# Kernel tuning notes

Hardware: AMD Instinct MI355X
Metric: run time of the kernel (lower is better)

Reference implementation:

```python
import jax, jax.numpy as jnp
import numpy as np

EPS = 1e-6        # eigenvalue clamp for numerical safety (matrices are well-conditioned by construction)
MOMENTUM = 0.1    # init kwarg


def _sym_apply(X, fn):
    """Apply a spectral function to a batch of symmetric matrices via eigh."""
    w, V = jnp.linalg.eigh(X)
    w = jnp.maximum(w, EPS)
    return jnp.einsum('...ij,...j,...kj->...ik', V, fn(w), V)


def sqrtm(X):
    return _sym_apply(X, jnp.sqrt)


def invsqrtm(X):
    return _sym_apply(X, lambda w: 1.0 / jnp.sqrt(w))


def logm(X):
    return _sym_apply(X, jnp.log)


def expm_sym(X):
    w, V = jnp.linalg.eigh(X)
    return jnp.einsum('...ij,...j,...kj->...ik', V, jnp.exp(w), V)


def powm(X, t):
    return _sym_apply(X, lambda w: w ** t)


def congr_neg(X, G):
    """CongrG(X, G, 'neg') = G^{-1/2} X G^{-1/2}, broadcast over batch dims of X."""
    Gi = invsqrtm(G)
    return jnp.einsum('ij,...jk,kl->...il', Gi, X, Gi)


def bary_geom(Xm):
    """Karcher (Frechet) mean of SPD matrices Xm: (N, n, n).
    One Karcher-flow step initialized at the arithmetic mean (SPDNet-BN convention)."""
    G = jnp.mean(Xm, axis=0)
    Gs, Gi = sqrtm(G), invsqrtm(G)
    L = logm(jnp.einsum('ij,bjk,kl->bil', Gi, Xm, Gi))   # log-maps at G
    return Gs @ expm_sym(jnp.mean(L, axis=0)) @ Gs


def geodesic(A, B, t):
    """SPD geodesic from A toward B at time t: A^{1/2} (A^{-1/2} B A^{-1/2})^t A^{1/2}."""
    As, Ai = sqrtm(A), invsqrtm(A)
    return As @ powm(Ai @ B @ Ai, t) @ As


def setup_inputs() -> dict:
    key = jax.random.key(0)
    N, T, V, M, n = 32, 64, 25, 2, 16
    A = jax.random.normal(key, (N, T, V, M, n, n), dtype=jnp.float32)
    # SPD construction: A A^T / n + 0.5 I  (min eigenvalue >= 0.5)
    X = jnp.einsum('...ij,...kj->...ik', A, A) / n + 0.5 * jnp.eye(n, dtype=jnp.float32)
    running_mean = jnp.eye(n, dtype=jnp.float32)  # torch.eye(n) in __init__
    return {"X": X, "running_mean": running_mean}


def reference(X, running_mean):
    N, T, V, M, n, _ = X.shape
    Xf = X.reshape(N, T * V * M, n, n)
    X_mean = jnp.mean(Xf, axis=1)                      # (N, n, n) per-sample arithmetic mean
    mean = bary_geom(X_mean)                           # (n, n) Karcher mean over batch
    new_running_mean = geodesic(running_mean, mean, MOMENTUM)  # no_grad EMA in torch
    X_centered = congr_neg(Xf, mean)                   # mean^{-1/2} X mean^{-1/2}
    return X_centered.reshape(N, T, V, M, n, n), new_running_mean
```

## Files before the change

kernel.cpp:

```cpp
#include <hip/hip_runtime.h>
#include <math.h>

#define NS     32
#define BBATCH 3200
#define NMAT   102400
#define EPSC   1e-6f
#define ST     20
#define IX(i,j) ((i)*ST+(j))
#define MSZ    (16*ST)

#define PART_O 0
#define XM_O   131072
#define GS_O   139264
#define GI_O   139520
#define L_O    139776
#define MEAN_O 147968
#define WI_O   148224
#define RS_O   148480
#define RI_O   148736


__device__ __forceinline__ void g2l(const float* __restrict__ g, float* l, int t) {
  if (t < 64) {
    int i = t >> 2, j0 = (t & 3) << 2;
    *(float4*)&l[IX(i, j0)] = *(const float4*)&g[i * 16 + j0];
  }
  __syncthreads();
}

__device__ __forceinline__ void l2g(const float* l, float* __restrict__ g, int t) {
  if (t < 64) {
    int i = t >> 2, j0 = (t & 3) << 2;
    *(float4*)&g[i * 16 + j0] = *(const float4*)&l[IX(i, j0)];
  }
  __syncthreads();
}

__device__ __forceinline__ void mm(const float* A, const float* B, float* C, int t) {
  if (t < 64) {
    int i = t >> 2, j0 = (t & 3) << 2;
    float4 acc = make_float4(0.f, 0.f, 0.f, 0.f);
    #pragma unroll
    for (int k = 0; k < 16; ++k) {
      float a = A[IX(i, k)];
      const float4 b = *(const float4*)&B[IX(k, j0)];
      acc.x += a * b.x; acc.y += a * b.y; acc.z += a * b.z; acc.w += a * b.w;
    }
    *(float4*)&C[IX(i, j0)] = acc;
  }
  __syncthreads();
}

__device__ __forceinline__ void mad_diag(float* C, float s, float d, int t) {
  if (t < 64) {
    int i = t >> 2, j0 = (t & 3) << 2;
    float4 p = *(float4*)&C[IX(i, j0)];
    p.x *= s; p.y *= s; p.z *= s; p.w *= s;
    if (i == j0) p.x += d; else if (i == j0 + 1) p.y += d;
    else if (i == j0 + 2) p.z += d; else if (i == j0 + 3) p.w += d;
    *(float4*)&C[IX(i, j0)] = p;
  }
  __syncthreads();
}

__device__ __forceinline__ void set_scaled_I(float* C, float d, int t) {
  if (t < 64) {
    int i = t >> 2, j0 = (t & 3) << 2;
    float4 p = make_float4(0.f, 0.f, 0.f, 0.f);
    if (i == j0) p.x = d; else if (i == j0 + 1) p.y = d;
    else if (i == j0 + 2) p.z = d; else if (i == j0 + 3) p.w = d;
    *(float4*)&C[IX(i, j0)] = p;
  }
  __syncthreads();
}

__device__ __forceinline__ void symmetrize(float* A, int t) {
  float4 v = make_float4(0.f, 0.f, 0.f, 0.f);
  if (t < 64) {
    int i = t >> 2, j0 = (t & 3) << 2;
    float4 a = *(float4*)&A[IX(i, j0)];
    v.x = 0.5f * (a.x + A[IX(j0,     i)]);
    v.y = 0.5f * (a.y + A[IX(j0 + 1, i)]);
    v.z = 0.5f * (a.z + A[IX(j0 + 2, i)]);
    v.w = 0.5f * (a.w + A[IX(j0 + 3, i)]);
  }
  __syncthreads();
  if (t < 64) {
    int i = t >> 2, j0 = (t & 3) << 2;
    *(float4*)&A[IX(i, j0)] = v;
  }
  __syncthreads();
}

__device__ __forceinline__ float trace16(const float* A) {
  float tr = 0.f;
  #pragma unroll
  for (int k = 0; k < 16; ++k) tr += A[IX(k, k)];
  return tr;
}

#define NS_IT 8
__device__ void ns_sqrtm(const float* A, float* Y0, float* Y1, float* Z0, float* Z1,
                         float* P, int t, float** pS, float** pZ) {
  float c = trace16(A) * (1.f / 16.f);
  float ic = 1.f / c;
  if (t < 64) {
    int i = t >> 2, j0 = (t & 3) << 2;
    float4 a = *(const float4*)&A[IX(i, j0)];
    a.x *= ic; a.y *= ic; a.z *= ic; a.w *= ic;
    *(float4*)&Y0[IX(i, j0)] = a;
    float4 z = make_float4(0.f, 0.f, 0.f, 0.f);
    if (i == j0) z.x = 1.f; else if (i == j0 + 1) z.y = 1.f;
    else if (i == j0 + 2) z.z = 1.f; else if (i == j0 + 3) z.w = 1.f;
    *(float4*)&Z0[IX(i, j0)] = z;
  }
  __syncthreads();
  float *Y = Y0, *Yn = Y1, *Z = Z0, *Zn = Z1;
  for (int it = 0; it < NS_IT; ++it) {
    mm(Z, Y, P, t);
    mad_diag(P, -0.5f, 1.5f, t);
    mm(Y, P, Yn, t);
    mm(P, Z, Zn, t);
    float* tp = Y; Y = Yn; Yn = tp;
    tp = Z; Z = Zn; Zn = tp;
  }
  float sc = sqrtf(c), isc = 1.f / sc;
  if (t < 64) {
    int i = t >> 2, j0 = (t & 3) << 2;
    float4 y = *(float4*)&Y[IX(i, j0)];
    y.x *= sc; y.y *= sc; y.z *= sc; y.w *= sc;
    *(float4*)&Y[IX(i, j0)] = y;
    float4 z = *(float4*)&Z[IX(i, j0)];
    z.x *= isc; z.y *= isc; z.z *= isc; z.w *= isc;
    *(float4*)&Z[IX(i, j0)] = z;
  }
  __syncthreads();
  *pS = Y; *pZ = Z;
}

#define LOG_M 12
__device__ void logm_taylor(float* S, float* L, float* R0, float* R1, int t) {
  mad_diag(S, 1.f, -1.f, t);
  float am = ((LOG_M & 1) ? 1.f : -1.f) / (float)LOG_M;
  set_scaled_I(R0, am, t);
  float *R = R0, *Rn = R1;
  for (int j = LOG_M - 1; j >= 1; --j) {
    mm(S, R, Rn, t);
    float aj = ((j & 1) ? 1.f : -1.f) / (float)j;
    mad_diag(Rn, 1.f, aj, t);
    float* tp = R; R = Rn; Rn = tp;
  }
  mm(S, R, L, t);
}

#define EXP_M 10
__device__ float* expm_taylor(const float* K, float* R0, float* R1, int t) {
  set_scaled_I(R0, 1.f, t);
  float *R = R0, *Rn = R1;
  for (int j = EXP_M; j >= 1; --j) {
    mm(K, R, Rn, t);
    mad_diag(Rn, 1.f / (float)j, 1.f, t);
    float* tp = R; R = Rn; Rn = tp;
  }
  return R;
}


__global__ __launch_bounds__(256) void k_part(const float* __restrict__ X, float* __restrict__ ws) {
  int b = blockIdx.x >> 4;
  int c = blockIdx.x & 15;
  int t = threadIdx.x;
  int e4 = t & 63;
  int r  = t >> 6;
  const float4* X4 = (const float4*)X;
  float4 s = make_float4(0.f, 0.f, 0.f, 0.f);
  long mbase = (long)b * BBATCH + c * 200;
  for (int i = r; i < 200; i += 4) {
    float4 v = X4[(mbase + i) * 64 + e4];
    s.x += v.x; s.y += v.y; s.z += v.z; s.w += v.w;
  }
  __shared__ float4 red[256];
  red[t] = s;
  __syncthreads();
  if (t < 64) {
    float4 a = red[t], b1 = red[t + 64], c1 = red[t + 128], d = red[t + 192];
    float4 o;
    o.x = a.x + b1.x + c1.x + d.x;
    o.y = a.y + b1.y + c1.y + d.y;
    o.z = a.z + b1.z + c1.z + d.z;
    o.w = a.w + b1.w + c1.w + d.w;
    ((float4*)(ws + PART_O))[(long)blockIdx.x * 64 + t] = o;
  }
}

__global__ __launch_bounds__(256) void k_xm(float* __restrict__ ws) {
  int b = blockIdx.x, t = threadIdx.x;
  float a = 0.f;
  for (int c = 0; c < 16; ++c) a += ws[PART_O + (b * 16 + c) * 256 + t];
  ws[XM_O + b * 256 + t] = a * (1.f / BBATCH);
}

__global__ __launch_bounds__(64) void k_prep(const float* __restrict__ rm, float* __restrict__ ws) {
  __shared__ __align__(16) float A[MSZ], Y0[MSZ], Y1[MSZ], Z0[MSZ], Z1[MSZ], P[MSZ];
  int t = threadIdx.x;
  if (blockIdx.x == 0) {
    if (t < 64) {
      int i = t >> 2, j0 = (t & 3) << 2;
      float4 a = make_float4(0.f, 0.f, 0.f, 0.f);
      for (int b = 0; b < NS; ++b) {
        float4 v = *(const float4*)&ws[XM_O + b * 256 + i * 16 + j0];
        a.x += v.x; a.y += v.y; a.z += v.z; a.w += v.w;
      }
      float s = 1.f / NS;
      a.x *= s; a.y *= s; a.z *= s; a.w *= s;
      *(float4*)&A[IX(i, j0)] = a;
    }
    __syncthreads();
  } else {
    g2l(rm, A, t);
  }
  float *S, *Z;
  ns_sqrtm(A, Y0, Y1, Z0, Z1, P, t, &S, &Z);
  l2g(S, ws + (blockIdx.x == 0 ? GS_O : RS_O), t);
  l2g(Z, ws + (blockIdx.x == 0 ? GI_O : RI_O), t);
}

__global__ __launch_bounds__(64) void k_logmap(float* __restrict__ ws) {
  __shared__ __align__(16) float Gi[MSZ], Xb[MSZ], S[MSZ], T[MSZ], R0[MSZ], R1[MSZ];
  int b = blockIdx.x, t = threadIdx.x;
  g2l(ws + GI_O, Gi, t);
  g2l(ws + XM_O + b * 256, Xb, t);
  mm(Gi, Xb, T, t);
  mm(T, Gi, S, t);
  symmetrize(S, t);
  logm_taylor(S, T, R0, R1, t);
  l2g(T, ws + L_O + b * 256, t);
}

__global__ __launch_bounds__(64) void k_mean2(float* __restrict__ ws) {
  __shared__ __align__(16) float K[MSZ], Gs[MSZ], T1[MSZ], T2[MSZ], R0[MSZ], R1[MSZ], P[MSZ];
  int t = threadIdx.x;
  if (t < 64) {
    int i = t >> 2, j0 = (t & 3) << 2;
    float4 a = make_float4(0.f, 0.f, 0.f, 0.f);
    for (int b = 0; b < NS; ++b) {
      float4 v = *(const float4*)&ws[L_O + b * 256 + i * 16 + j0];
      a.x += v.x; a.y += v.y; a.z += v.z; a.w += v.w;
    }
    float s = 1.f / NS;
    a.x *= s; a.y *= s; a.z *= s; a.w *= s;
    *(float4*)&K[IX(i, j0)] = a;
  }
  __syncthreads();
  float* E = expm_taylor(K, R0, R1, t);
  g2l(ws + GS_O, Gs, t);
  mm(Gs, E, T1, t);
  mm(T1, Gs, T2, t);
  symmetrize(T2, t);
  l2g(T2, ws + MEAN_O, t);
  float *S, *Z;
  ns_sqrtm(T2, R0, R1, T1, K, P, t, &S, &Z);
  l2g(Z, ws + WI_O, t);
}

__global__ __launch_bounds__(256) void k_center(const float* __restrict__ X,
                                                const float* __restrict__ ws,
                                                float* __restrict__ out) {
  __shared__ __align__(16) float B0[MSZ], B1[MSZ], B2[MSZ], B3[MSZ], B4[MSZ];
  __shared__ __align__(16) float Xs[4 * MSZ];
  __shared__ __align__(16) float Ts[4 * MSZ];
  __shared__ __align__(16) float Wsm[MSZ];
  int t = threadIdx.x;

  if (blockIdx.x == 0) {
    g2l(ws + RI_O, B0, t);
    g2l(ws + MEAN_O, B1, t);
    mm(B0, B1, B2, t);
    mm(B2, B0, B1, t);
    symmetrize(B1, t);
    float c = trace16(B1) * (1.f / 16.f);
    mad_diag(B1, 1.f / c, 0.f, t);
    logm_taylor(B1, B2, B3, B4, t);
    mad_diag(B2, 0.1f, 0.f, t);
    float* Ep = expm_taylor(B2, B3, B4, t);
    float s = expf(0.1f * logf(c));
    mad_diag(Ep, s, 0.f, t);
    g2l(ws + RS_O, B1, t);
    mm(B1, Ep, B2, t);
    mm(B2, B1, B4, t);
    l2g(B4, out + (size_t)NMAT * 256, t);
  } else {
    long m0 = (long)(blockIdx.x - 1) * 4;
    Wsm[(t >> 4) * ST + (t & 15)] = ws[WI_O + t];
    const float4* X4 = (const float4*)X;
    float4 xv = X4[m0 * 64 + t];
    int mm_ = t >> 6;
    int l  = t & 63;
    int i  = l >> 2;
    int j0 = (l & 3) << 2;
    *(float4*)&Xs[mm_ * MSZ + i * ST + j0] = xv;
    __syncthreads();
    float4 a = make_float4(0.f, 0.f, 0.f, 0.f);
    #pragma unroll
    for (int k = 0; k < 16; ++k) {
      float x = Xs[mm_ * MSZ + i * ST + k];
      const float4 wv = *(const float4*)&Wsm[k * ST + j0];
      a.x += x * wv.x; a.y += x * wv.y; a.z += x * wv.z; a.w += x * wv.w;
    }
    *(float4*)&Ts[mm_ * MSZ + i * ST + j0] = a;
    __syncthreads();
    float4 y = make_float4(0.f, 0.f, 0.f, 0.f);
    #pragma unroll
    for (int k = 0; k < 16; ++k) {
      float w = Wsm[i * ST + k];
      const float4 tv = *(const float4*)&Ts[mm_ * MSZ + k * ST + j0];
      y.x += w * tv.x; y.y += w * tv.y; y.z += w * tv.z; y.w += w * tv.w;
    }
    ((float4*)out)[m0 * 64 + t] = y;
  }
}

extern "C" void kernel_launch(void* const* d_in, const int* in_sizes, int n_in,
                              void* d_out, int out_size, void* d_ws, size_t ws_size,
                              hipStream_t stream) {
  (void)in_sizes; (void)n_in; (void)out_size; (void)ws_size;
  const float* X  = (const float*)d_in[0];
  const float* rm = (const float*)d_in[1];
  float* out = (float*)d_out;
  float* ws  = (float*)d_ws;

  k_part   <<<dim3(512),   dim3(256), 0, stream>>>(X, ws);
  k_xm     <<<dim3(32),    dim3(256), 0, stream>>>(ws);
  k_prep   <<<dim3(2),     dim3(64),  0, stream>>>(rm, ws);
  k_logmap <<<dim3(32),    dim3(64),  0, stream>>>(ws);
  k_mean2  <<<dim3(1),     dim3(64),  0, stream>>>(ws);
  k_center <<<dim3(25601), dim3(256), 0, stream>>>(X, ws, out);
}
```

Before: 246.4 us.

## Fuse spectral stages into one wave-synchronous kernel and restructure centering

Merges the four small serial kernels (mean reduction, sqrt prep, log-maps, Karcher mean, geodesic) into a single 256-thread block. Each wavefront works independently and uses LDS waitcnt in place of block barriers, which cuts launch and barrier overhead on the serial critical path. Newton-Schulz and Taylor iteration counts are reduced, which may hurt accuracy. The centering kernel now processes 16 matrices per block with register-held W rows and prefetch of the next X matrix.

```diff
diff --git a/kernel.cpp b/kernel.cpp
--- a/kernel.cpp
+++ b/kernel.cpp
@@ -4,162 +4,152 @@
 #define NS     32
 #define BBATCH 3200
 #define NMAT   102400
-#define EPSC   1e-6f
 #define ST     20
 #define IX(i,j) ((i)*ST+(j))
 #define MSZ    (16*ST)
+#define SLAB   324
 
 #define PART_O 0
 #define XM_O   131072
-#define GS_O   139264
-#define GI_O   139520
-#define L_O    139776
-#define MEAN_O 147968
-#define WI_O   148224
-#define RS_O   148480
-#define RI_O   148736
-
-
-__device__ __forceinline__ void g2l(const float* __restrict__ g, float* l, int t) {
-  if (t < 64) {
-    int i = t >> 2, j0 = (t & 3) << 2;
-    *(float4*)&l[IX(i, j0)] = *(const float4*)&g[i * 16 + j0];
-  }
-  __syncthreads();
-}
-
-__device__ __forceinline__ void l2g(const float* l, float* __restrict__ g, int t) {
-  if (t < 64) {
-    int i = t >> 2, j0 = (t & 3) << 2;
-    *(float4*)&g[i * 16 + j0] = *(const float4*)&l[IX(i, j0)];
-  }
-  __syncthreads();
-}
-
-__device__ __forceinline__ void mm(const float* A, const float* B, float* C, int t) {
-  if (t < 64) {
-    int i = t >> 2, j0 = (t & 3) << 2;
-    float4 acc = make_float4(0.f, 0.f, 0.f, 0.f);
-    #pragma unroll
-    for (int k = 0; k < 16; ++k) {
-      float a = A[IX(i, k)];
-      const float4 b = *(const float4*)&B[IX(k, j0)];
-      acc.x += a * b.x; acc.y += a * b.y; acc.z += a * b.z; acc.w += a * b.w;
-    }
-    *(float4*)&C[IX(i, j0)] = acc;
-  }
-  __syncthreads();
-}
-
-__device__ __forceinline__ void mad_diag(float* C, float s, float d, int t) {
-  if (t < 64) {
-    int i = t >> 2, j0 = (t & 3) << 2;
-    float4 p = *(float4*)&C[IX(i, j0)];
-    p.x *= s; p.y *= s; p.z *= s; p.w *= s;
-    if (i == j0) p.x += d; else if (i == j0 + 1) p.y += d;
-    else if (i == j0 + 2) p.z += d; else if (i == j0 + 3) p.w += d;
-    *(float4*)&C[IX(i, j0)] = p;
-  }
-  __syncthreads();
-}
-
-__device__ __forceinline__ void set_scaled_I(float* C, float d, int t) {
-  if (t < 64) {
-    int i = t >> 2, j0 = (t & 3) << 2;
-    float4 p = make_float4(0.f, 0.f, 0.f, 0.f);
-    if (i == j0) p.x = d; else if (i == j0 + 1) p.y = d;
-    else if (i == j0 + 2) p.z = d; else if (i == j0 + 3) p.w = d;
-    *(float4*)&C[IX(i, j0)] = p;
-  }
-  __syncthreads();
-}
-
-__device__ __forceinline__ void symmetrize(float* A, int t) {
-  float4 v = make_float4(0.f, 0.f, 0.f, 0.f);
-  if (t < 64) {
-    int i = t >> 2, j0 = (t & 3) << 2;
-    float4 a = *(float4*)&A[IX(i, j0)];
-    v.x = 0.5f * (a.x + A[IX(j0,     i)]);
-    v.y = 0.5f * (a.y + A[IX(j0 + 1, i)]);
-    v.z = 0.5f * (a.z + A[IX(j0 + 2, i)]);
-    v.w = 0.5f * (a.w + A[IX(j0 + 3, i)]);
-  }
-  __syncthreads();
-  if (t < 64) {
-    int i = t >> 2, j0 = (t & 3) << 2;
-    *(float4*)&A[IX(i, j0)] = v;
-  }
-  __syncthreads();
-}
-
-__device__ __forceinline__ float trace16(const float* A) {
+#define WI_O   139264
+
+#define NS_IT  5
+#define LOG_M  8
+#define EXP_M  8
+
+
+__device__ __forceinline__ void wsync() {
+  asm volatile("s_waitcnt lgkmcnt(0)" ::: "memory");
+}
+
+__device__ __forceinline__ void g2l_w(const float* __restrict__ g, float* L, int l) {
+  int i = l >> 2, j0 = (l & 3) << 2;
+  *(float4*)&L[IX(i, j0)] = *(const float4*)&g[i * 16 + j0];
+  wsync();
+}
+
+__device__ __forceinline__ void l2g_w(const float* L, float* __restrict__ g, int l) {
+  int i = l >> 2, j0 = (l & 3) << 2;
+  *(float4*)&g[i * 16 + j0] = *(const float4*)&L[IX(i, j0)];
+}
+
+__device__ __forceinline__ void cpy_w(const float* S, float* D, int l) {
+  int i = l >> 2, j0 = (l & 3) << 2;
+  float4 v = *(const float4*)&S[IX(i, j0)];
+  wsync();
+  *(float4*)&D[IX(i, j0)] = v;
+  wsync();
+}
+
+__device__ __forceinline__ void mm_w(const float* A, const float* B, float* C, int l) {
+  int i = l >> 2, j0 = (l & 3) << 2;
+  float4 acc = make_float4(0.f, 0.f, 0.f, 0.f);
+  #pragma unroll
+  for (int k = 0; k < 16; ++k) {
+    float a = A[IX(i, k)];
+    float4 b = *(const float4*)&B[IX(k, j0)];
+    acc.x += a * b.x; acc.y += a * b.y; acc.z += a * b.z; acc.w += a * b.w;
+  }
+  wsync();
+  *(float4*)&C[IX(i, j0)] = acc;
+  wsync();
+}
+
+__device__ __forceinline__ void mad_diag_w(float* C, float s, float d, int l) {
+  int i = l >> 2, j0 = (l & 3) << 2;
+  float4 p = *(float4*)&C[IX(i, j0)];
+  p.x *= s; p.y *= s; p.z *= s; p.w *= s;
+  if (i == j0) p.x += d; else if (i == j0 + 1) p.y += d;
+  else if (i == j0 + 2) p.z += d; else if (i == j0 + 3) p.w += d;
+  wsync();
+  *(float4*)&C[IX(i, j0)] = p;
+  wsync();
+}
+
+__device__ __forceinline__ void setI_w(float* C, float d, int l) {
+  int i = l >> 2, j0 = (l & 3) << 2;
+  float4 p = make_float4(0.f, 0.f, 0.f, 0.f);
+  if (i == j0) p.x = d; else if (i == j0 + 1) p.y = d;
+  else if (i == j0 + 2) p.z = d; else if (i == j0 + 3) p.w = d;
+  *(float4*)&C[IX(i, j0)] = p;
+  wsync();
+}
+
+__device__ __forceinline__ void add_w(float* D, const float* S, int l) {
+  int i = l >> 2, j0 = (l & 3) << 2;
+  float4 d = *(float4*)&D[IX(i, j0)];
+  float4 s = *(const float4*)&S[IX(i, j0)];
+  d.x += s.x; d.y += s.y; d.z += s.z; d.w += s.w;
+  wsync();
+  *(float4*)&D[IX(i, j0)] = d;
+  wsync();
+}
+
+__device__ __forceinline__ void sym_w(float* A, int l) {
+  int i = l >> 2, j0 = (l & 3) << 2;
+  float4 a = *(float4*)&A[IX(i, j0)];
+  float4 v;
+  v.x = 0.5f * (a.x + A[IX(j0,     i)]);
+  v.y = 0.5f * (a.y + A[IX(j0 + 1, i)]);
+  v.z = 0.5f * (a.z + A[IX(j0 + 2, i)]);
+  v.w = 0.5f * (a.w + A[IX(j0 + 3, i)]);
+  wsync();
+  *(float4*)&A[IX(i, j0)] = v;
+  wsync();
+}
+
+__device__ __forceinline__ float trace16_w(const float* A) {
   float tr = 0.f;
   #pragma unroll
   for (int k = 0; k < 16; ++k) tr += A[IX(k, k)];
   return tr;
 }
 
-#define NS_IT 8
-__device__ void ns_sqrtm(const float* A, float* Y0, float* Y1, float* Z0, float* Z1,
-                         float* P, int t, float** pS, float** pZ) {
-  float c = trace16(A) * (1.f / 16.f);
+__device__ void ns_sqrtm_w(const float* A, float* Y0, float* Y1, float* Z0, float* Z1,
+                           float* P, int l, float** pS, float** pZ) {
+  float c = trace16_w(A) * (1.f / 16.f);
   float ic = 1.f / c;
-  if (t < 64) {
-    int i = t >> 2, j0 = (t & 3) << 2;
+  {
+    int i = l >> 2, j0 = (l & 3) << 2;
     float4 a = *(const float4*)&A[IX(i, j0)];
     a.x *= ic; a.y *= ic; a.z *= ic; a.w *= ic;
     *(float4*)&Y0[IX(i, j0)] = a;
-    float4 z = make_float4(0.f, 0.f, 0.f, 0.f);
-    if (i == j0) z.x = 1.f; else if (i == j0 + 1) z.y = 1.f;
-    else if (i == j0 + 2) z.z = 1.f; else if (i == j0 + 3) z.w = 1.f;
-    *(float4*)&Z0[IX(i, j0)] = z;
-  }
-  __syncthreads();
+  }
+  setI_w(Z0, 1.f, l);
   float *Y = Y0, *Yn = Y1, *Z = Z0, *Zn = Z1;
   for (int it = 0; it < NS_IT; ++it) {
-    mm(Z, Y, P, t);
-    mad_diag(P, -0.5f, 1.5f, t);
-    mm(Y, P, Yn, t);
-    mm(P, Z, Zn, t);
+    mm_w(Z, Y, P, l);
+    mad_diag_w(P, -0.5f, 1.5f, l);
+    mm_w(Y, P, Yn, l);
+    mm_w(P, Z, Zn, l);
     float* tp = Y; Y = Yn; Yn = tp;
     tp = Z; Z = Zn; Zn = tp;
   }
-  float sc = sqrtf(c), isc = 1.f / sc;
-  if (t < 64) {
-    int i = t >> 2, j0 = (t & 3) << 2;
-    float4 y = *(float4*)&Y[IX(i, j0)];
-    y.x *= sc; y.y *= sc; y.z *= sc; y.w *= sc;
-    *(float4*)&Y[IX(i, j0)] = y;
-    float4 z = *(float4*)&Z[IX(i, j0)];
-    z.x *= isc; z.y *= isc; z.z *= isc; z.w *= isc;
-    *(float4*)&Z[IX(i, j0)] = z;
-  }
-  __syncthreads();
+  mad_diag_w(Y, sqrtf(c), 0.f, l);
+  mad_diag_w(Z, 1.f / sqrtf(c), 0.f, l);
   *pS = Y; *pZ = Z;
 }
 
-#define LOG_M 12
-__device__ void logm_taylor(float* S, float* L, float* R0, float* R1, int t) {
-  mad_diag(S, 1.f, -1.f, t);
+__device__ void logm_w(float* S, float* L, float* R0, float* R1, int l) {
+  mad_diag_w(S, 1.f, -1.f, l);
   float am = ((LOG_M & 1) ? 1.f : -1.f) / (float)LOG_M;
-  set_scaled_I(R0, am, t);
+  setI_w(R0, am, l);
   float *R = R0, *Rn = R1;
   for (int j = LOG_M - 1; j >= 1; --j) {
-    mm(S, R, Rn, t);
+    mm_w(S, R, Rn, l);
     float aj = ((j & 1) ? 1.f : -1.f) / (float)j;
-    mad_diag(Rn, 1.f, aj, t);
+    mad_diag_w(Rn, 1.f, aj, l);
     float* tp = R; R = Rn; Rn = tp;
   }
-  mm(S, R, L, t);
-}
-
-#define EXP_M 10
-__device__ float* expm_taylor(const float* K, float* R0, float* R1, int t) {
-  set_scaled_I(R0, 1.f, t);
+  mm_w(S, R, L, l);
+}
+
+__device__ float* expm_w(const float* K, float* R0, float* R1, int l) {
+  setI_w(R0, 1.f, l);
   float *R = R0, *Rn = R1;
   for (int j = EXP_M; j >= 1; --j) {
-    mm(K, R, Rn, t);
-    mad_diag(Rn, 1.f / (float)j, 1.f, t);
+    mm_w(K, R, Rn, l);
+    mad_diag_w(Rn, 1.f / (float)j, 1.f, l);
     float* tp = R; R = Rn; Rn = tp;
   }
   return R;
@@ -193,130 +183,169 @@
   }
 }
 
-__global__ __launch_bounds__(256) void k_xm(float* __restrict__ ws) {
-  int b = blockIdx.x, t = threadIdx.x;
-  float a = 0.f;
-  for (int c = 0; c < 16; ++c) a += ws[PART_O + (b * 16 + c) * 256 + t];
-  ws[XM_O + b * 256 + t] = a * (1.f / BBATCH);
-}
-
-__global__ __launch_bounds__(64) void k_prep(const float* __restrict__ rm, float* __restrict__ ws) {
-  __shared__ __align__(16) float A[MSZ], Y0[MSZ], Y1[MSZ], Z0[MSZ], Z1[MSZ], P[MSZ];
-  int t = threadIdx.x;
-  if (blockIdx.x == 0) {
-    if (t < 64) {
-      int i = t >> 2, j0 = (t & 3) << 2;
+__global__ __launch_bounds__(256) void k_spectral(const float* __restrict__ rm,
+                                                  float* __restrict__ ws,
+                                                  float* __restrict__ out) {
+  __shared__ __align__(16) float shA[5 * MSZ];
+  __shared__ __align__(16) float wb[4][6 * MSZ];
+  int t = threadIdx.x, w = t >> 6, l = t & 63;
+  float* Gi = &shA[0];
+  float* Gs = &shA[MSZ];
+  float* Ri = &shA[2 * MSZ];
+  float* Rs = &shA[3 * MSZ];
+
+  for (int o = t; o < NS * 256; o += 256) {
+    int b = o >> 8, e = o & 255;
+    float a = 0.f;
+    for (int c = 0; c < 16; ++c) a += ws[PART_O + (b * 16 + c) * 256 + e];
+    ws[XM_O + o] = a * (1.f / BBATCH);
+  }
+  __threadfence_block();
+  __syncthreads();
+
+  if (w == 0) {
+    float* B = wb[0];
+    int i = l >> 2, j0 = (l & 3) << 2;
+    float4 a = make_float4(0.f, 0.f, 0.f, 0.f);
+    for (int b = 0; b < NS; ++b) {
+      float4 v = *(const float4*)&ws[XM_O + b * 256 + i * 16 + j0];
+      a.x += v.x; a.y += v.y; a.z += v.z; a.w += v.w;
+    }
+    float s = 1.f / NS;
+    a.x *= s; a.y *= s; a.z *= s; a.w *= s;
+    *(float4*)&B[IX(i, j0)] = a;
+    wsync();
+    float *S, *Z;
+    ns_sqrtm_w(B, B + MSZ, B + 2 * MSZ, B + 3 * MSZ, B + 4 * MSZ, B + 5 * MSZ, l, &S, &Z);
+    cpy_w(S, Gs, l);
+    cpy_w(Z, Gi, l);
+  } else if (w == 1) {
+    float* B = wb[1];
+    g2l_w(rm, B, l);
+    float *S, *Z;
+    ns_sqrtm_w(B, B + MSZ, B + 2 * MSZ, B + 3 * MSZ, B + 4 * MSZ, B + 5 * MSZ, l, &S, &Z);
+    cpy_w(S, Rs, l);
+    cpy_w(Z, Ri, l);
+  }
+  __syncthreads();
+
+  {
+    float* c0 = wb[w];
+    float* c1 = wb[w] + MSZ;
+    float* c2 = wb[w] + 2 * MSZ;
+    float* c3 = wb[w] + 3 * MSZ;
+    float* c4 = wb[w] + 4 * MSZ;
+    float* c5 = wb[w] + 5 * MSZ;
+    setI_w(c5, 0.f, l);
+    for (int r = 0; r < 8; ++r) {
+      int b = w * 8 + r;
+      g2l_w(ws + XM_O + b * 256, c0, l);
+      mm_w(Gi, c0, c1, l);
+      mm_w(c1, Gi, c2, l);
+      sym_w(c2, l);
+      logm_w(c2, c1, c3, c4, l);
+      add_w(c5, c1, l);
+    }
+  }
+  __syncthreads();
+
+  if (w == 0) {
+    float* b0 = wb[0];
+    float* b1 = wb[0] + MSZ;
+    float* b2 = wb[0] + 2 * MSZ;
+    float* b3 = wb[0] + 3 * MSZ;
+    float* b4 = wb[0] + 4 * MSZ;
+    float* b5 = wb[0] + 5 * MSZ;
+    {
+      int i = l >> 2, j0 = (l & 3) << 2;
       float4 a = make_float4(0.f, 0.f, 0.f, 0.f);
-      for (int b = 0; b < NS; ++b) {
-        float4 v = *(const float4*)&ws[XM_O + b * 256 + i * 16 + j0];
+      #pragma unroll
+      for (int q = 0; q < 4; ++q) {
+        float4 v = *(const float4*)&wb[q][5 * MSZ + IX(i, j0)];
         a.x += v.x; a.y += v.y; a.z += v.z; a.w += v.w;
       }
       float s = 1.f / NS;
       a.x *= s; a.y *= s; a.z *= s; a.w *= s;
-      *(float4*)&A[IX(i, j0)] = a;
-    }
-    __syncthreads();
-  } else {
-    g2l(rm, A, t);
-  }
-  float *S, *Z;
-  ns_sqrtm(A, Y0, Y1, Z0, Z1, P, t, &S, &Z);
-  l2g(S, ws + (blockIdx.x == 0 ? GS_O : RS_O), t);
-  l2g(Z, ws + (blockIdx.x == 0 ? GI_O : RI_O), t);
-}
-
-__global__ __launch_bounds__(64) void k_logmap(float* __restrict__ ws) {
-  __shared__ __align__(16) float Gi[MSZ], Xb[MSZ], S[MSZ], T[MSZ], R0[MSZ], R1[MSZ];
-  int b = blockIdx.x, t = threadIdx.x;
-  g2l(ws + GI_O, Gi, t);
-  g2l(ws + XM_O + b * 256, Xb, t);
-  mm(Gi, Xb, T, t);
-  mm(T, Gi, S, t);
-  symmetrize(S, t);
-  logm_taylor(S, T, R0, R1, t);
-  l2g(T, ws + L_O + b * 256, t);
-}
-
-__global__ __launch_bounds__(64) void k_mean2(float* __restrict__ ws) {
-  __shared__ __align__(16) float K[MSZ], Gs[MSZ], T1[MSZ], T2[MSZ], R0[MSZ], R1[MSZ], P[MSZ];
-  int t = threadIdx.x;
-  if (t < 64) {
-    int i = t >> 2, j0 = (t & 3) << 2;
-    float4 a = make_float4(0.f, 0.f, 0.f, 0.f);
-    for (int b = 0; b < NS; ++b) {
-      float4 v = *(const float4*)&ws[L_O + b * 256 + i * 16 + j0];
-      a.x += v.x; a.y += v.y; a.z += v.z; a.w += v.w;
-    }
-    float s = 1.f / NS;
-    a.x *= s; a.y *= s; a.z *= s; a.w *= s;
-    *(float4*)&K[IX(i, j0)] = a;
-  }
-  __syncthreads();
-  float* E = expm_taylor(K, R0, R1, t);
-  g2l(ws + GS_O, Gs, t);
-  mm(Gs, E, T1, t);
-  mm(T1, Gs, T2, t);
-  symmetrize(T2, t);
-  l2g(T2, ws + MEAN_O, t);
-  float *S, *Z;
-  ns_sqrtm(T2, R0, R1, T1, K, P, t, &S, &Z);
-  l2g(Z, ws + WI_O, t);
+      wsync();
+      *(float4*)&b0[IX(i, j0)] = a;
+      wsync();
+    }
+    float* E = expm_w(b0, b1, b2, l);
+    mm_w(Gs, E, b3, l);
+    mm_w(b3, Gs, b4, l);
+    sym_w(b4, l);
+    float *S, *Z;
+    ns_sqrtm_w(b4, b0, b1, b2, b3, b5, l, &S, &Z);
+    l2g_w(Z, ws + WI_O, l);
+    mm_w(Ri, b4, b0, l);
+    mm_w(b0, Ri, b1, l);
+    sym_w(b1, l);
+    float c = trace16_w(b1) * (1.f / 16.f);
+    mad_diag_w(b1, 1.f / c, 0.f, l);
+    logm_w(b1, b0, b2, b3, l);
+    mad_diag_w(b0, 0.1f, 0.f, l);
+    float* E2 = expm_w(b0, b1, b2, l);
+    mad_diag_w(E2, expf(0.1f * logf(c)), 0.f, l);
+    mm_w(Rs, E2, b3, l);
+    mm_w(b3, Rs, b0, l);
+    l2g_w(b0, out + (size_t)NMAT * 256, l);
+  }
 }
 
 __global__ __launch_bounds__(256) void k_center(const float* __restrict__ X,
                                                 const float* __restrict__ ws,
                                                 float* __restrict__ out) {
-  __shared__ __align__(16) float B0[MSZ], B1[MSZ], B2[MSZ], B3[MSZ], B4[MSZ];
-  __shared__ __align__(16) float Xs[4 * MSZ];
-  __shared__ __align__(16) float Ts[4 * MSZ];
-  __shared__ __align__(16) float Wsm[MSZ];
-  int t = threadIdx.x;
-
-  if (blockIdx.x == 0) {
-    g2l(ws + RI_O, B0, t);
-    g2l(ws + MEAN_O, B1, t);
-    mm(B0, B1, B2, t);
-    mm(B2, B0, B1, t);
-    symmetrize(B1, t);
-    float c = trace16(B1) * (1.f / 16.f);
-    mad_diag(B1, 1.f / c, 0.f, t);
-    logm_taylor(B1, B2, B3, B4, t);
-    mad_diag(B2, 0.1f, 0.f, t);
-    float* Ep = expm_taylor(B2, B3, B4, t);
-    float s = expf(0.1f * logf(c));
-    mad_diag(Ep, s, 0.f, t);
-    g2l(ws + RS_O, B1, t);
-    mm(B1, Ep, B2, t);
-    mm(B2, B1, B4, t);
-    l2g(B4, out + (size_t)NMAT * 256, t);
-  } else {
-    long m0 = (long)(blockIdx.x - 1) * 4;
-    Wsm[(t >> 4) * ST + (t & 15)] = ws[WI_O + t];
-    const float4* X4 = (const float4*)X;
-    float4 xv = X4[m0 * 64 + t];
-    int mm_ = t >> 6;
-    int l  = t & 63;
-    int i  = l >> 2;
-    int j0 = (l & 3) << 2;
-    *(float4*)&Xs[mm_ * MSZ + i * ST + j0] = xv;
-    __syncthreads();
-    float4 a = make_float4(0.f, 0.f, 0.f, 0.f);
+  __shared__ __align__(16) float Wl[MSZ];
+  __shared__ __align__(16) float sX[4][SLAB];
+  __shared__ __align__(16) float sU[4][SLAB];
+  int t = threadIdx.x, w = t >> 6, l = t & 63;
+  int i = l >> 2, j0 = (l & 3) << 2;
+
+  *(float4*)&Wl[IX(l >> 2, (l & 3) << 2)] = ((const float4*)(ws + WI_O))[l];
+  wsync();
+
+  float wr[16];
+  #pragma unroll
+  for (int c = 0; c < 4; ++c) {
+    float4 v = *(const float4*)&Wl[IX(i, 4 * c)];
+    wr[4 * c] = v.x; wr[4 * c + 1] = v.y; wr[4 * c + 2] = v.z; wr[4 * c + 3] = v.w;
+  }
+
+  long base = (long)blockIdx.x * 16 + w * 4;
+  const float4* X4 = (const float4*)X;
+  float4* O4 = (float4*)out;
+
+  float4 xv = X4[base * 64 + l];
+  #pragma unroll
+  for (int it = 0; it < 4; ++it) {
+    float4 xn = make_float4(0.f, 0.f, 0.f, 0.f);
+    if (it < 3) xn = X4[(base + it + 1) * 64 + l];
+    *(float4*)&sX[w][IX(i, j0)] = xv;
+    wsync();
+    float4 u = make_float4(0.f, 0.f, 0.f, 0.f);
     #pragma unroll
     for (int k = 0; k < 16; ++k) {
-      float x = Xs[mm_ * MSZ + i * ST + k];
-      const float4 wv = *(const float4*)&Wsm[k * ST + j0];
-      a.x += x * wv.x; a.y += x * wv.y; a.z += x * wv.z; a.w += x * wv.w;
-    }
-    *(float4*)&Ts[mm_ * MSZ + i * ST + j0] = a;
-    __syncthreads();
+      float4 b = *(const float4*)&sX[w][IX(k, j0)];
+      float a = wr[k];
+      u.x += a * b.x; u.y += a * b.y; u.z += a * b.z; u.w += a * b.w;
+    }
+    *(float4*)&sU[w][IX(i, j0)] = u;
+    wsync();
+    float ur[16];
+    #pragma unroll
+    for (int c = 0; c < 4; ++c) {
+      float4 v = *(const float4*)&sU[w][IX(i, 4 * c)];
+      ur[4 * c] = v.x; ur[4 * c + 1] = v.y; ur[4 * c + 2] = v.z; ur[4 * c + 3] = v.w;
+    }
     float4 y = make_float4(0.f, 0.f, 0.f, 0.f);
     #pragma unroll
     for (int k = 0; k < 16; ++k) {
-      float w = Wsm[i * ST + k];
-      const float4 tv = *(const float4*)&Ts[mm_ * MSZ + k * ST + j0];
-      y.x += w * tv.x; y.y += w * tv.y; y.z += w * tv.z; y.w += w * tv.w;
-    }
-    ((float4*)out)[m0 * 64 + t] = y;
+      float4 b = *(const float4*)&Wl[IX(k, j0)];
+      float a = ur[k];
+      y.x += a * b.x; y.y += a * b.y; y.z += a * b.z; y.w += a * b.w;
+    }
+    O4[(base + it) * 64 + l] = y;
+    xv = xn;
   }
 }
 
@@ -329,10 +358,7 @@
   float* out = (float*)d_out;
   float* ws  = (float*)d_ws;
 
-  k_part   <<<dim3(512),   dim3(256), 0, stream>>>(X, ws);
-  k_xm     <<<dim3(32),    dim3(256), 0, stream>>>(ws);
-  k_prep   <<<dim3(2),     dim3(64),  0, stream>>>(rm, ws);
-  k_logmap <<<dim3(32),    dim3(64),  0, stream>>>(ws);
-  k_mean2  <<<dim3(1),     dim3(64),  0, stream>>>(ws);
-  k_center <<<dim3(25601), dim3(256), 0, stream>>>(X, ws, out);
-}
+  k_part     <<<dim3(512),  dim3(256), 0, stream>>>(X, ws);
+  k_spectral <<<dim3(1),    dim3(256), 0, stream>>>(rm, ws, out);
+  k_center   <<<dim3(6400), dim3(256), 0, stream>>>(X, ws, out);
+}
```

After: 274.8 us. 1.12x slower.
